# Kernel optimization log

Hardware: AMD Instinct MI355X
Metric: run time of the kernel (lower is better)

The kernel has to match this reference:

```python
import jax, jax.numpy as jnp
import numpy as np

B, L, V, A = 4096, 64, 50000, 1000
E, H, G, F2 = 32, 32, 256, 512


def _xavier(k, shape):
    fan_out, fan_in = shape
    a = np.sqrt(6.0 / (fan_in + fan_out)).astype(np.float32)
    return jax.random.uniform(k, shape, jnp.float32, -a, a)


def setup_inputs() -> dict:
    key = jax.random.key(0)
    ks = jax.random.split(key, 32)
    inp = {}
    inp["q"] = jax.random.randint(ks[0], (B, L), 0, V)
    for i in range(8):
        inp[f"sf{i}"] = jax.random.randint(ks[1 + i], (B, L), 0, V)
    inp["emb"] = _xavier(ks[9], (V, E))
    # torch LSTM weight layout: [4H, in] with gate order i,f,g,o; biases init to 0
    inp["q_Wih"] = _xavier(ks[10], (4 * H, E))
    inp["q_Whh"] = _xavier(ks[11], (4 * H, H))
    inp["q_b"] = jnp.zeros((4 * H,), jnp.float32)
    inp["sf_Wih"] = _xavier(ks[12], (4 * H, E))
    inp["sf_Whh"] = _xavier(ks[13], (4 * H, H))
    inp["sf_b"] = jnp.zeros((4 * H,), jnp.float32)
    inp["g1_W"] = _xavier(ks[14], (G, 2 * H + 1)); inp["g1_b"] = jnp.zeros((G,), jnp.float32)
    inp["g2_W"] = _xavier(ks[15], (G, G)); inp["g2_b"] = jnp.zeros((G,), jnp.float32)
    inp["g3_W"] = _xavier(ks[16], (G, G)); inp["g3_b"] = jnp.zeros((G,), jnp.float32)
    inp["g4_W"] = _xavier(ks[17], (G, G)); inp["g4_b"] = jnp.zeros((G,), jnp.float32)
    inp["f1_W"] = _xavier(ks[18], (G, G)); inp["f1_b"] = jnp.zeros((G,), jnp.float32)
    inp["f2_W"] = _xavier(ks[19], (F2, G)); inp["f2_b"] = jnp.zeros((F2,), jnp.float32)
    inp["f3_W"] = _xavier(ks[20], (A, F2)); inp["f3_b"] = jnp.zeros((A,), jnp.float32)
    return inp


def _lstm_last(x, Wih, Whh, b):
    """x: [L, N, E] -> final hidden state [N, H]. Torch gate order i,f,g,o."""
    n = x.shape[1]
    h_dim = Whh.shape[1]
    def step(carry, xt):
        h, c = carry
        gates = xt @ Wih.T + h @ Whh.T + b  # [N, 4H]
        i, f, g, o = jnp.split(gates, 4, axis=-1)
        c = jax.nn.sigmoid(f) * c + jax.nn.sigmoid(i) * jnp.tanh(g)
        h = jax.nn.sigmoid(o) * jnp.tanh(c)
        return (h, c), None
    init = (jnp.zeros((n, h_dim), x.dtype), jnp.zeros((n, h_dim), x.dtype))
    (h, _), _ = jax.lax.scan(step, init, x)
    return h


def _lin(x, W, b):
    return x @ W.T + b


def reference(q, sf0, sf1, sf2, sf3, sf4, sf5, sf6, sf7,
              emb, q_Wih, q_Whh, q_b, sf_Wih, sf_Whh, sf_b,
              g1_W, g1_b, g2_W, g2_b, g3_W, g3_b, g4_W, g4_b,
              f1_W, f1_b, f2_W, f2_b, f3_W, f3_b):
    # dropout in eval mode (identity)
    b, l = q.shape
    qe = emb[q].transpose(1, 0, 2)  # [L, B, E]
    hq = _lstm_last(qe, q_Wih, q_Whh, q_b)  # [B, H]

    sf = jnp.stack([sf0, sf1, sf2, sf3, sf4, sf5, sf6, sf7])  # [8, B, L]
    sfe = emb[sf]  # [8, B, L, E]
    sfe = sfe.transpose(2, 0, 1, 3).reshape(l, 8 * b, emb.shape[1])  # one fused LSTM over 8*B
    hs = _lstm_last(sfe, sf_Wih, sf_Whh, sf_b).reshape(8, b, -1)  # [8, B, H]

    pos = jnp.broadcast_to(jnp.arange(8, dtype=hs.dtype)[:, None, None], (8, b, 1))
    x = jnp.concatenate([hs, jnp.broadcast_to(hq, (8, b, hq.shape[-1])), pos], axis=-1)  # [8, B, 65]
    x = jax.nn.relu(_lin(x, g1_W, g1_b))
    x = jax.nn.relu(_lin(x, g2_W, g2_b))
    x = jax.nn.relu(_lin(x, g3_W, g3_b))
    x = jax.nn.relu(_lin(x, g4_W, g4_b))
    g_o = x.sum(axis=0)  # [B, 256] segment-sum over the 8 relations

    x = jax.nn.relu(_lin(g_o, f1_W, f1_b))
    x = jax.nn.relu(_lin(x, f2_W, f2_b))
    return _lin(x, f3_W, f3_b)  # [B, A]
```

## Files before the change

kernel.cpp:

```cpp
#include <hip/hip_runtime.h>
#include <stdint.h>
#include <stddef.h>

typedef __fp16 f16;
typedef __attribute__((ext_vector_type(8))) __fp16 half8;
typedef __attribute__((ext_vector_type(4))) __fp16 half4;
typedef __attribute__((ext_vector_type(4))) float f32x4;
typedef unsigned int u32;

static __device__ __forceinline__ f32x4 mfma16(half8 a, half8 b, f32x4 c) {
    return __builtin_amdgcn_mfma_f32_16x16x32_f16(a, b, c, 0, 0, 0);
}
static __device__ __forceinline__ float fexp2(float x) { float r; asm("v_exp_f32 %0, %1" : "=v"(r) : "v"(x)); return r; }
static __device__ __forceinline__ float frcp(float x)  { float r; asm("v_rcp_f32 %0, %1" : "=v"(r) : "v"(x)); return r; }

static constexpr float L2E  = 1.4426950408889634f;
static constexpr float L2E2 = 2.8853900817779268f;

static constexpr int LDA = 264;
static constexpr int LDF2 = 520;

static constexpr size_t OFF_EMB   = 0;
static constexpr size_t OFF_WQIH  = 3200000;
static constexpr size_t OFF_WQHH  = OFF_WQIH + 8192;
static constexpr size_t OFF_WSIH  = OFF_WQHH + 8192;
static constexpr size_t OFF_WSHH  = OFF_WSIH + 8192;
static constexpr size_t OFF_BQ    = OFF_WSHH + 8192;
static constexpr size_t OFF_BS    = OFF_BQ + 512;
static constexpr size_t OFF_G1WP  = OFF_BS + 512;
static constexpr size_t OFF_BIAS8 = OFF_G1WP + 32768;
static constexpr size_t OFF_G2W   = OFF_BIAS8 + 8192;
static constexpr size_t OFF_G3W   = OFF_G2W + 131072;
static constexpr size_t OFF_G4W   = OFF_G3W + 131072;
static constexpr size_t OFF_F1W   = OFF_G4W + 131072;
static constexpr size_t OFF_F2W   = OFF_F1W + 131072;
static constexpr size_t OFF_F3W   = OFF_F2W + 262144;
static constexpr size_t OFF_HS    = OFF_F3W + 1024000;
static constexpr size_t OFF_HQ    = OFF_HS + 2097152;
static constexpr size_t OFF_ACT2  = OFF_HQ + 262144;
static constexpr size_t WS_NEED   = OFF_ACT2 + 16777216;

struct CvtJobs { const float* src[7]; f16* dst[7]; int n[7]; };

__global__ __launch_bounds__(256) void cvt_prep(
    CvtJobs j,
    const float* __restrict__ g1W, const float* __restrict__ g1b,
    f16* __restrict__ wp, float* __restrict__ bias8,
    const float* __restrict__ qWih, const float* __restrict__ qWhh, const float* __restrict__ qb,
    const float* __restrict__ sWih, const float* __restrict__ sWhh, const float* __restrict__ sb,
    f16* __restrict__ wqih, f16* __restrict__ wqhh, float* __restrict__ bq,
    f16* __restrict__ wsih, f16* __restrict__ wshh, float* __restrict__ bs)
{
    int t = threadIdx.x;
    if (blockIdx.y < 7) {
        int jb = blockIdx.y;
        int i = (blockIdx.x * 256 + t) * 8;
        if (i >= j.n[jb]) return;
        const float* s = j.src[jb] + i;
        f32x4 a = *(const f32x4*)s;
        f32x4 b = *(const f32x4*)(s + 4);
        half8 o;
        o[0]=(f16)a[0]; o[1]=(f16)a[1]; o[2]=(f16)a[2]; o[3]=(f16)a[3];
        o[4]=(f16)b[0]; o[5]=(f16)b[1]; o[6]=(f16)b[2]; o[7]=(f16)b[3];
        *(half8*)(j.dst[jb] + i) = o;
        return;
    }
    if (blockIdx.x == 0) {
        int col = t;
        for (int k = 0; k < 64; k++) wp[col * 64 + k] = (f16)g1W[col * 65 + k];
        float wpos = g1W[col * 65 + 64];
        float b = g1b[col];
        for (int i = 0; i < 8; i++) bias8[i * 256 + col] = b + (float)i * wpos;
    } else if (blockIdx.x == 1) {
        for (int i = t; i < 4096; i += 256) {
            int row = i >> 5;
            float s = (row < 64 || row >= 96) ? -L2E : L2E2;
            wqih[i] = (f16)(qWih[i] * s);
            wqhh[i] = (f16)(qWhh[i] * s);
            wsih[i] = (f16)(sWih[i] * s);
            wshh[i] = (f16)(sWhh[i] * s);
        }
        if (t < 128) {
            float s = (t < 64 || t >= 96) ? -L2E : L2E2;
            bq[t] = qb[t] * s;
            bs[t] = sb[t] * s;
        }
    }
}

struct SfPtrs { const int* p[8]; };

__global__ __launch_bounds__(128) void lstm_kernel(
    SfPtrs sf, const int* __restrict__ qtok, const f16* __restrict__ emb_h,
    const f16* __restrict__ wih_sf, const f16* __restrict__ whh_sf, const float* __restrict__ b_sf,
    const f16* __restrict__ wih_q,  const f16* __restrict__ whh_q,  const float* __restrict__ b_q,
    f16* __restrict__ hs_out, f16* __restrict__ hq_out)
{
    __shared__ __align__(16) char hbuf[2][16 * 80];
    int tid = threadIdx.x;
    int w = tid >> 6, lane = tid & 63;
    int c15 = lane & 15, kq = lane >> 4;
    int sbase = blockIdx.x * 16;
    bool isq = sbase >= 32768;
    const f16* wih = isq ? wih_q : wih_sf;
    const f16* whh = isq ? whh_q : whh_sf;
    const float* bvec = isq ? b_q : b_sf;

    half8 wi[4], wh[4];
    f32x4 bc[4];
    #pragma unroll
    for (int jg = 0; jg < 4; jg++) {
        int row = (2 * jg + w) * 16 + c15;
        wi[jg] = *(const half8*)(wih + row * 32 + kq * 8);
        wh[jg] = *(const half8*)(whh + row * 32 + kq * 8);
        bc[jg] = *(const f32x4*)(bvec + (2 * jg + w) * 16 + kq * 4);
    }
    int sg = sbase + c15;
    const int* tp;
    if (isq) tp = qtok + (sg - 32768) * 64;
    else     tp = sf.p[sg >> 12] + (sg & 4095) * 64;

    for (int i = tid; i < 640; i += 128) ((u32*)hbuf[0])[i] = 0;
    __syncthreads();

    float cst[4] = {};
    int rb = 0;
    const int hoff_r = c15 * 80 + kq * 16;
    const int hoff_w = c15 * 80 + w * 32 + kq * 8;

    half8 xf = *(const half8*)(emb_h + (size_t)tp[0] * 32 + kq * 8);

    #pragma unroll 1
    for (int t = 0; t < 64; t++) {
        half8 hf = *(const half8*)(hbuf[rb] + hoff_r);
        f32x4 acc[4];
        #pragma unroll
        for (int jg = 0; jg < 4; jg++) acc[jg] = mfma16(wi[jg], xf, bc[jg]);
        #pragma unroll
        for (int jg = 0; jg < 4; jg++) acc[jg] = mfma16(wh[jg], hf, acc[jg]);
        if (t < 63) {
            int tk = tp[t + 1];
            xf = *(const half8*)(emb_h + (size_t)tk * 32 + kq * 8);
        }
        half4 hp;
        #pragma unroll
        for (int r = 0; r < 4; r++) {
            float ei = fexp2(acc[0][r]);
            float ef = fexp2(acc[1][r]);
            float eg = fexp2(acc[2][r]);
            float eo = fexp2(acc[3][r]);
            float t1 = 1.f + ei, t2 = 1.f + ef, t5 = 1.f + eo;
            float eg1 = eg + 1.f, egm = eg - 1.f;
            float t1e = t1 * eg1;
            float num = fmaf(egm, t2, cst[r] * t1e);
            float cn  = num * frcp(t1e * t2);
            cst[r] = cn;
            float ec  = fexp2(cn * L2E2);
            hp[r] = (f16)((ec - 1.f) * frcp((ec + 1.f) * t5));
        }
        *(half4*)(hbuf[rb ^ 1] + hoff_w) = hp;
        __syncthreads();
        rb ^= 1;
    }
    if (w == 0) {
        half8 hv = *(const half8*)(hbuf[rb] + hoff_r);
        if (isq) *(half8*)(hq_out + (size_t)(sg - 32768) * 32 + kq * 8) = hv;
        else     *(half8*)(hs_out + (size_t)sg * 32 + kq * 8) = hv;
    }
}

template<bool TOGLOBAL>
static __device__ __forceinline__ void layer256(
    const f16 (* __restrict__ src)[LDA], f16 (* __restrict__ dst)[LDA],
    const f16* __restrict__ W, const float* __restrict__ bias,
    f16* __restrict__ gout, int m0, int wm, int wn, int c15, int kq)
{
    f32x4 acc[2][4];
    #pragma unroll
    for (int a = 0; a < 2; a++)
        #pragma unroll
        for (int b = 0; b < 4; b++) acc[a][b] = (f32x4){0.f, 0.f, 0.f, 0.f};
    #pragma unroll
    for (int k0 = 0; k0 < 8; k0++) {
        half8 av[2], bv[4];
        #pragma unroll
        for (int fm = 0; fm < 2; fm++) av[fm] = *(const half8*)(&src[wm * 32 + fm * 16 + c15][k0 * 32 + kq * 8]);
        #pragma unroll
        for (int fn = 0; fn < 4; fn++) bv[fn] = *(const half8*)(W + (size_t)(wn * 64 + fn * 16 + c15) * 256 + k0 * 32 + kq * 8);
        #pragma unroll
        for (int fm = 0; fm < 2; fm++)
            #pragma unroll
            for (int fn = 0; fn < 4; fn++) acc[fm][fn] = mfma16(av[fm], bv[fn], acc[fm][fn]);
    }
    #pragma unroll
    for (int fn = 0; fn < 4; fn++) {
        int col = wn * 64 + fn * 16 + c15;
        float bb = bias[col];
        #pragma unroll
        for (int fm = 0; fm < 2; fm++)
            #pragma unroll
            for (int r = 0; r < 4; r++) {
                float v = fmaxf(acc[fm][fn][r] + bb, 0.f);
                int row = wm * 32 + fm * 16 + kq * 4 + r;
                if (TOGLOBAL) gout[(size_t)(m0 + row) * 256 + col] = (f16)v;
                else          dst[row][col] = (f16)v;
            }
    }
}

__global__ __launch_bounds__(512) void gemm_g1234(
    const f16* __restrict__ hs, const f16* __restrict__ hq,
    const f16* __restrict__ g1wp, const float* __restrict__ bias8,
    const f16* __restrict__ g2w, const float* __restrict__ g2b,
    const f16* __restrict__ g3w, const float* __restrict__ g3b,
    const f16* __restrict__ g4w, const float* __restrict__ g4b,
    f16* __restrict__ act2)
{
    __shared__ __align__(16) f16 actA[64][LDA];
    __shared__ __align__(16) f16 actB[64][LDA];
    const int wv = threadIdx.x >> 6, lane = threadIdx.x & 63;
    const int c15 = lane & 15, kq = lane >> 4;
    const int wm = wv >> 2, wn = wv & 3;
    const int m0 = blockIdx.x * 64;
    const float* brow = bias8 + ((m0 >> 12) << 8);

    {
        f32x4 acc[2][4];
        #pragma unroll
        for (int a = 0; a < 2; a++)
            #pragma unroll
            for (int b = 0; b < 4; b++) acc[a][b] = (f32x4){0.f, 0.f, 0.f, 0.f};
        half8 av[2], bv[4];
        #pragma unroll
        for (int fm = 0; fm < 2; fm++) av[fm] = *(const half8*)(hs + (size_t)(m0 + wm * 32 + fm * 16 + c15) * 32 + kq * 8);
        #pragma unroll
        for (int fn = 0; fn < 4; fn++) bv[fn] = *(const half8*)(g1wp + (size_t)(wn * 64 + fn * 16 + c15) * 64 + kq * 8);
        #pragma unroll
        for (int fm = 0; fm < 2; fm++)
            #pragma unroll
            for (int fn = 0; fn < 4; fn++) acc[fm][fn] = mfma16(av[fm], bv[fn], acc[fm][fn]);
        #pragma unroll
        for (int fm = 0; fm < 2; fm++) av[fm] = *(const half8*)(hq + (size_t)((m0 + wm * 32 + fm * 16 + c15) & 4095) * 32 + kq * 8);
        #pragma unroll
        for (int fn = 0; fn < 4; fn++) bv[fn] = *(const half8*)(g1wp + (size_t)(wn * 64 + fn * 16 + c15) * 64 + 32 + kq * 8);
        #pragma unroll
        for (int fm = 0; fm < 2; fm++)
            #pragma unroll
            for (int fn = 0; fn < 4; fn++) acc[fm][fn] = mfma16(av[fm], bv[fn], acc[fm][fn]);
        #pragma unroll
        for (int fn = 0; fn < 4; fn++) {
            int col = wn * 64 + fn * 16 + c15;
            float bb = brow[col];
            #pragma unroll
            for (int fm = 0; fm < 2; fm++)
                #pragma unroll
                for (int r = 0; r < 4; r++)
                    actA[wm * 32 + fm * 16 + kq * 4 + r][col] = (f16)fmaxf(acc[fm][fn][r] + bb, 0.f);
        }
    }
    __syncthreads();
    layer256<false>(actA, actB, g2w, g2b, nullptr, m0, wm, wn, c15, kq);
    __syncthreads();
    layer256<false>(actB, actA, g3w, g3b, nullptr, m0, wm, wn, c15, kq);
    __syncthreads();
    layer256<true>(actA, actB, g4w, g4b, act2, m0, wm, wn, c15, kq);
}

__global__ __launch_bounds__(512) void f123s_kernel(
    const f16* __restrict__ act2,
    const f16* __restrict__ f1w, const float* __restrict__ f1b,
    const f16* __restrict__ f2w, const float* __restrict__ f2b,
    const f16* __restrict__ f3w, const float* __restrict__ f3b,
    float* __restrict__ out)
{
    __shared__ __align__(16) f16 smbuf[16][LDA];
    __shared__ __align__(16) f16 f1buf[16][LDA];
    __shared__ __align__(16) f16 f2buf[16][LDF2];
    const int b0 = blockIdx.x * 16;

    {
        int r = threadIdx.x >> 5, cb = (threadIdx.x & 31) * 8;
        float s[8] = {};
        #pragma unroll
        for (int i = 0; i < 8; i++) {
            half8 v = *(const half8*)(act2 + ((size_t)(i * 4096 + b0 + r)) * 256 + cb);
            #pragma unroll
            for (int q = 0; q < 8; q++) s[q] += (float)v[q];
        }
        half8 o;
        #pragma unroll
        for (int q = 0; q < 8; q++) o[q] = (f16)s[q];
        *(half8*)(&smbuf[r][cb]) = o;
    }
    __syncthreads();
    const int wv = threadIdx.x >> 6, lane = threadIdx.x & 63;
    const int c15 = lane & 15, kq = lane >> 4;

    {
        f32x4 acc[2];
        acc[0] = (f32x4){0.f, 0.f, 0.f, 0.f}; acc[1] = acc[0];
        #pragma unroll
        for (int k0 = 0; k0 < 8; k0++) {
            half8 a = *(const half8*)(&smbuf[c15][k0 * 32 + kq * 8]);
            #pragma unroll
            for (int fn = 0; fn < 2; fn++) {
                half8 bv = *(const half8*)(f1w + (size_t)(wv * 32 + fn * 16 + c15) * 256 + k0 * 32 + kq * 8);
                acc[fn] = mfma16(a, bv, acc[fn]);
            }
        }
        #pragma unroll
        for (int fn = 0; fn < 2; fn++) {
            int col = wv * 32 + fn * 16 + c15;
            float bb = f1b[col];
            #pragma unroll
            for (int r = 0; r < 4; r++)
                f1buf[kq * 4 + r][col] = (f16)fmaxf(acc[fn][r] + bb, 0.f);
        }
    }
    __syncthreads();
    {
        f32x4 acc[4];
        #pragma unroll
        for (int b = 0; b < 4; b++) acc[b] = (f32x4){0.f, 0.f, 0.f, 0.f};
        #pragma unroll
        for (int k0 = 0; k0 < 8; k0++) {
            half8 a = *(const half8*)(&f1buf[c15][k0 * 32 + kq * 8]);
            #pragma unroll
            for (int fn = 0; fn < 4; fn++) {
                half8 bv = *(const half8*)(f2w + (size_t)(wv * 64 + fn * 16 + c15) * 256 + k0 * 32 + kq * 8);
                acc[fn] = mfma16(a, bv, acc[fn]);
            }
        }
        #pragma unroll
        for (int fn = 0; fn < 4; fn++) {
            int col = wv * 64 + fn * 16 + c15;
            float bb = f2b[col];
            #pragma unroll
            for (int r = 0; r < 4; r++)
                f2buf[kq * 4 + r][col] = (f16)fmaxf(acc[fn][r] + bb, 0.f);
        }
    }
    __syncthreads();
    {
        f32x4 acc[8];
        #pragma unroll
        for (int b = 0; b < 8; b++) acc[b] = (f32x4){0.f, 0.f, 0.f, 0.f};
        #pragma unroll
        for (int k0 = 0; k0 < 16; k0++) {
            half8 a = *(const half8*)(&f2buf[c15][k0 * 32 + kq * 8]);
            #pragma unroll
            for (int fn = 0; fn < 8; fn++) {
                int col = wv * 128 + fn * 16 + c15;
                int cl = col < 1000 ? col : 999;
                half8 bv = *(const half8*)(f3w + (size_t)cl * 512 + k0 * 32 + kq * 8);
                acc[fn] = mfma16(a, bv, acc[fn]);
            }
        }
        #pragma unroll
        for (int fn = 0; fn < 8; fn++) {
            int col = wv * 128 + fn * 16 + c15;
            if (col < 1000) {
                float bb = f3b[col];
                #pragma unroll
                for (int r = 0; r < 4; r++)
                    out[(size_t)(b0 + kq * 4 + r) * 1000 + col] = acc[fn][r] + bb;
            }
        }
    }
}

extern "C" void kernel_launch(void* const* d_in, const int* in_sizes, int n_in,
                              void* d_out, int out_size, void* d_ws, size_t ws_size,
                              hipStream_t stream)
{
    if (ws_size < WS_NEED) return;
    const int* q_tok = (const int*)d_in[0];
    SfPtrs sf;
    for (int i = 0; i < 8; i++) sf.p[i] = (const int*)d_in[1 + i];
    const float* emb_f = (const float*)d_in[9];
    const float* qWih = (const float*)d_in[10];
    const float* qWhh = (const float*)d_in[11];
    const float* q_b  = (const float*)d_in[12];
    const float* sWih = (const float*)d_in[13];
    const float* sWhh = (const float*)d_in[14];
    const float* s_b  = (const float*)d_in[15];
    const float* g1W  = (const float*)d_in[16];
    const float* g1b  = (const float*)d_in[17];
    const float* g2W  = (const float*)d_in[18];
    const float* g2b  = (const float*)d_in[19];
    const float* g3W  = (const float*)d_in[20];
    const float* g3b  = (const float*)d_in[21];
    const float* g4W  = (const float*)d_in[22];
    const float* g4b  = (const float*)d_in[23];
    const float* f1W  = (const float*)d_in[24];
    const float* f1b  = (const float*)d_in[25];
    const float* f2W  = (const float*)d_in[26];
    const float* f2b  = (const float*)d_in[27];
    const float* f3W  = (const float*)d_in[28];
    const float* f3b  = (const float*)d_in[29];

    char* ws = (char*)d_ws;
    f16* emb_h = (f16*)(ws + OFF_EMB);
    f16* wqih  = (f16*)(ws + OFF_WQIH);
    f16* wqhh  = (f16*)(ws + OFF_WQHH);
    f16* wsih  = (f16*)(ws + OFF_WSIH);
    f16* wshh  = (f16*)(ws + OFF_WSHH);
    float* bq  = (float*)(ws + OFF_BQ);
    float* bs  = (float*)(ws + OFF_BS);
    f16* g1wp  = (f16*)(ws + OFF_G1WP);
    float* bias8 = (float*)(ws + OFF_BIAS8);
    f16* g2w = (f16*)(ws + OFF_G2W);
    f16* g3w = (f16*)(ws + OFF_G3W);
    f16* g4w = (f16*)(ws + OFF_G4W);
    f16* f1w = (f16*)(ws + OFF_F1W);
    f16* f2w = (f16*)(ws + OFF_F2W);
    f16* f3w = (f16*)(ws + OFF_F3W);
    f16* hs  = (f16*)(ws + OFF_HS);
    f16* hq  = (f16*)(ws + OFF_HQ);
    f16* act2 = (f16*)(ws + OFF_ACT2);

    CvtJobs cj;
    const float* srcs[7] = {emb_f, g2W, g3W, g4W, f1W, f2W, f3W};
    f16* dsts[7]         = {emb_h, g2w, g3w, g4w, f1w, f2w, f3w};
    int ns[7] = {1600000, 65536, 65536, 65536, 65536, 131072, 512000};
    for (int i = 0; i < 7; i++) { cj.src[i] = srcs[i]; cj.dst[i] = dsts[i]; cj.n[i] = ns[i]; }

    cvt_prep<<<dim3(782, 8), 256, 0, stream>>>(cj, g1W, g1b, g1wp, bias8,
                                               qWih, qWhh, q_b, sWih, sWhh, s_b,
                                               wqih, wqhh, bq, wsih, wshh, bs);
    lstm_kernel<<<2304, 128, 0, stream>>>(sf, q_tok, emb_h, wsih, wshh, bs, wqih, wqhh, bq, hs, hq);
    gemm_g1234<<<512, 512, 0, stream>>>(hs, hq, g1wp, bias8, g2w, g2b, g3w, g3b, g4w, g4b, act2);
    f123s_kernel<<<256, 512, 0, stream>>>(act2, f1w, f1b, f2w, f2b, f3w, f3b, (float*)d_out);
}
```

Baseline: 319.5 us.

## Fuse relation sum into g-MLP kernel by regrouping rows per batch element

The g1-g4 kernel now assigns each block 8 batch elements across all 8 relations, so the segment-sum over relations happens in shared memory and only a [B,256] result goes to global memory instead of the [8B,256] activation buffer. The hq operand is loaded once per block because it is shared across relations. The downstream f1-f3 kernel now reads the pre-summed rows and runs with 1024 threads, splitting each layer's output columns across twice as many waves. Each block's hs loads become strided across relations, and the summed g_o is rounded to fp16 before f1.

```diff
diff --git a/kernel.cpp b/kernel.cpp
--- a/kernel.cpp
+++ b/kernel.cpp
@@ -37,8 +37,8 @@
 static constexpr size_t OFF_F3W   = OFF_F2W + 262144;
 static constexpr size_t OFF_HS    = OFF_F3W + 1024000;
 static constexpr size_t OFF_HQ    = OFF_HS + 2097152;
-static constexpr size_t OFF_ACT2  = OFF_HQ + 262144;
-static constexpr size_t WS_NEED   = OFF_ACT2 + 16777216;
+static constexpr size_t OFF_GO    = OFF_HQ + 262144;
+static constexpr size_t WS_NEED   = OFF_GO + 2097152;
 
 struct CvtJobs { const float* src[7]; f16* dst[7]; int n[7]; };
 
@@ -173,7 +173,7 @@
 static __device__ __forceinline__ void layer256(
     const f16 (* __restrict__ src)[LDA], f16 (* __restrict__ dst)[LDA],
     const f16* __restrict__ W, const float* __restrict__ bias,
-    f16* __restrict__ gout, int m0, int wm, int wn, int c15, int kq)
+    int wm, int wn, int c15, int kq)
 {
     f32x4 acc[2][4];
     #pragma unroll
@@ -201,9 +201,7 @@
             #pragma unroll
             for (int r = 0; r < 4; r++) {
                 float v = fmaxf(acc[fm][fn][r] + bb, 0.f);
-                int row = wm * 32 + fm * 16 + kq * 4 + r;
-                if (TOGLOBAL) gout[(size_t)(m0 + row) * 256 + col] = (f16)v;
-                else          dst[row][col] = (f16)v;
+                dst[wm * 32 + fm * 16 + kq * 4 + r][col] = (f16)v;
             }
     }
 }
@@ -214,15 +212,14 @@
     const f16* __restrict__ g2w, const float* __restrict__ g2b,
     const f16* __restrict__ g3w, const float* __restrict__ g3b,
     const f16* __restrict__ g4w, const float* __restrict__ g4b,
-    f16* __restrict__ act2)
+    f16* __restrict__ go)
 {
     __shared__ __align__(16) f16 actA[64][LDA];
     __shared__ __align__(16) f16 actB[64][LDA];
     const int wv = threadIdx.x >> 6, lane = threadIdx.x & 63;
     const int c15 = lane & 15, kq = lane >> 4;
     const int wm = wv >> 2, wn = wv & 3;
-    const int m0 = blockIdx.x * 64;
-    const float* brow = bias8 + ((m0 >> 12) << 8);
+    const int b8 = blockIdx.x * 8;
 
     {
         f32x4 acc[2][4];
@@ -231,8 +228,13 @@
             #pragma unroll
             for (int b = 0; b < 4; b++) acc[a][b] = (f32x4){0.f, 0.f, 0.f, 0.f};
         half8 av[2], bv[4];
-        #pragma unroll
-        for (int fm = 0; fm < 2; fm++) av[fm] = *(const half8*)(hs + (size_t)(m0 + wm * 32 + fm * 16 + c15) * 32 + kq * 8);
+        half8 avq = *(const half8*)(hq + (size_t)(b8 + (c15 & 7)) * 32 + kq * 8);
+        #pragma unroll
+        for (int fm = 0; fm < 2; fm++) {
+            int l = wm * 32 + fm * 16 + c15;
+            int rowg = (l >> 3) * 4096 + b8 + (l & 7);
+            av[fm] = *(const half8*)(hs + (size_t)rowg * 32 + kq * 8);
+        }
         #pragma unroll
         for (int fn = 0; fn < 4; fn++) bv[fn] = *(const half8*)(g1wp + (size_t)(wn * 64 + fn * 16 + c15) * 64 + kq * 8);
         #pragma unroll
@@ -240,34 +242,45 @@
             #pragma unroll
             for (int fn = 0; fn < 4; fn++) acc[fm][fn] = mfma16(av[fm], bv[fn], acc[fm][fn]);
         #pragma unroll
-        for (int fm = 0; fm < 2; fm++) av[fm] = *(const half8*)(hq + (size_t)((m0 + wm * 32 + fm * 16 + c15) & 4095) * 32 + kq * 8);
-        #pragma unroll
         for (int fn = 0; fn < 4; fn++) bv[fn] = *(const half8*)(g1wp + (size_t)(wn * 64 + fn * 16 + c15) * 64 + 32 + kq * 8);
         #pragma unroll
         for (int fm = 0; fm < 2; fm++)
             #pragma unroll
-            for (int fn = 0; fn < 4; fn++) acc[fm][fn] = mfma16(av[fm], bv[fn], acc[fm][fn]);
+            for (int fn = 0; fn < 4; fn++) acc[fm][fn] = mfma16(avq, bv[fn], acc[fm][fn]);
         #pragma unroll
         for (int fn = 0; fn < 4; fn++) {
             int col = wn * 64 + fn * 16 + c15;
-            float bb = brow[col];
-            #pragma unroll
-            for (int fm = 0; fm < 2; fm++)
+            #pragma unroll
+            for (int fm = 0; fm < 2; fm++) {
+                int rel = wm * 4 + fm * 2 + (kq >> 1);
+                float bb = bias8[rel * 256 + col];
                 #pragma unroll
                 for (int r = 0; r < 4; r++)
                     actA[wm * 32 + fm * 16 + kq * 4 + r][col] = (f16)fmaxf(acc[fm][fn][r] + bb, 0.f);
-        }
-    }
-    __syncthreads();
-    layer256<false>(actA, actB, g2w, g2b, nullptr, m0, wm, wn, c15, kq);
-    __syncthreads();
-    layer256<false>(actB, actA, g3w, g3b, nullptr, m0, wm, wn, c15, kq);
-    __syncthreads();
-    layer256<true>(actA, actB, g4w, g4b, act2, m0, wm, wn, c15, kq);
-}
-
-__global__ __launch_bounds__(512) void f123s_kernel(
-    const f16* __restrict__ act2,
+            }
+        }
+    }
+    __syncthreads();
+    layer256<false>(actA, actB, g2w, g2b, wm, wn, c15, kq);
+    __syncthreads();
+    layer256<false>(actB, actA, g3w, g3b, wm, wn, c15, kq);
+    __syncthreads();
+    layer256<false>(actA, actB, g4w, g4b, wm, wn, c15, kq);
+    __syncthreads();
+    {
+        float s0 = 0.f, s1 = 0.f, s2 = 0.f, s3 = 0.f;
+        #pragma unroll
+        for (int rel = 0; rel < 8; rel++) {
+            half4 v = *(const half4*)(&actB[rel * 8 + wv][lane * 4]);
+            s0 += (float)v[0]; s1 += (float)v[1]; s2 += (float)v[2]; s3 += (float)v[3];
+        }
+        half4 o; o[0] = (f16)s0; o[1] = (f16)s1; o[2] = (f16)s2; o[3] = (f16)s3;
+        *(half4*)(go + (size_t)(b8 + wv) * 256 + lane * 4) = o;
+    }
+}
+
+__global__ __launch_bounds__(1024) void f123s_kernel(
+    const f16* __restrict__ go,
     const f16* __restrict__ f1w, const float* __restrict__ f1b,
     const f16* __restrict__ f2w, const float* __restrict__ f2b,
     const f16* __restrict__ f3w, const float* __restrict__ f3b,
@@ -279,61 +292,46 @@
     const int b0 = blockIdx.x * 16;
 
     {
-        int r = threadIdx.x >> 5, cb = (threadIdx.x & 31) * 8;
-        float s[8] = {};
-        #pragma unroll
-        for (int i = 0; i < 8; i++) {
-            half8 v = *(const half8*)(act2 + ((size_t)(i * 4096 + b0 + r)) * 256 + cb);
-            #pragma unroll
-            for (int q = 0; q < 8; q++) s[q] += (float)v[q];
-        }
-        half8 o;
-        #pragma unroll
-        for (int q = 0; q < 8; q++) o[q] = (f16)s[q];
-        *(half8*)(&smbuf[r][cb]) = o;
+        int t = threadIdx.x;
+        if (t < 512) {
+            int r = t >> 5, cb = (t & 31) * 8;
+            *(half8*)(&smbuf[r][cb]) = *(const half8*)(go + (size_t)(b0 + r) * 256 + cb);
+        }
     }
     __syncthreads();
     const int wv = threadIdx.x >> 6, lane = threadIdx.x & 63;
     const int c15 = lane & 15, kq = lane >> 4;
 
     {
+        f32x4 acc = (f32x4){0.f, 0.f, 0.f, 0.f};
+        #pragma unroll
+        for (int k0 = 0; k0 < 8; k0++) {
+            half8 a = *(const half8*)(&smbuf[c15][k0 * 32 + kq * 8]);
+            half8 bv = *(const half8*)(f1w + (size_t)(wv * 16 + c15) * 256 + k0 * 32 + kq * 8);
+            acc = mfma16(a, bv, acc);
+        }
+        int col = wv * 16 + c15;
+        float bb = f1b[col];
+        #pragma unroll
+        for (int r = 0; r < 4; r++)
+            f1buf[kq * 4 + r][col] = (f16)fmaxf(acc[r] + bb, 0.f);
+    }
+    __syncthreads();
+    {
         f32x4 acc[2];
         acc[0] = (f32x4){0.f, 0.f, 0.f, 0.f}; acc[1] = acc[0];
         #pragma unroll
         for (int k0 = 0; k0 < 8; k0++) {
-            half8 a = *(const half8*)(&smbuf[c15][k0 * 32 + kq * 8]);
+            half8 a = *(const half8*)(&f1buf[c15][k0 * 32 + kq * 8]);
             #pragma unroll
             for (int fn = 0; fn < 2; fn++) {
-                half8 bv = *(const half8*)(f1w + (size_t)(wv * 32 + fn * 16 + c15) * 256 + k0 * 32 + kq * 8);
+                half8 bv = *(const half8*)(f2w + (size_t)(wv * 32 + fn * 16 + c15) * 256 + k0 * 32 + kq * 8);
                 acc[fn] = mfma16(a, bv, acc[fn]);
             }
         }
         #pragma unroll
         for (int fn = 0; fn < 2; fn++) {
             int col = wv * 32 + fn * 16 + c15;
-            float bb = f1b[col];
-            #pragma unroll
-            for (int r = 0; r < 4; r++)
-                f1buf[kq * 4 + r][col] = (f16)fmaxf(acc[fn][r] + bb, 0.f);
-        }
-    }
-    __syncthreads();
-    {
-        f32x4 acc[4];
-        #pragma unroll
-        for (int b = 0; b < 4; b++) acc[b] = (f32x4){0.f, 0.f, 0.f, 0.f};
-        #pragma unroll
-        for (int k0 = 0; k0 < 8; k0++) {
-            half8 a = *(const half8*)(&f1buf[c15][k0 * 32 + kq * 8]);
-            #pragma unroll
-            for (int fn = 0; fn < 4; fn++) {
-                half8 bv = *(const half8*)(f2w + (size_t)(wv * 64 + fn * 16 + c15) * 256 + k0 * 32 + kq * 8);
-                acc[fn] = mfma16(a, bv, acc[fn]);
-            }
-        }
-        #pragma unroll
-        for (int fn = 0; fn < 4; fn++) {
-            int col = wv * 64 + fn * 16 + c15;
             float bb = f2b[col];
             #pragma unroll
             for (int r = 0; r < 4; r++)
@@ -342,23 +340,23 @@
     }
     __syncthreads();
     {
-        f32x4 acc[8];
-        #pragma unroll
-        for (int b = 0; b < 8; b++) acc[b] = (f32x4){0.f, 0.f, 0.f, 0.f};
+        f32x4 acc[4];
+        #pragma unroll
+        for (int b = 0; b < 4; b++) acc[b] = (f32x4){0.f, 0.f, 0.f, 0.f};
         #pragma unroll
         for (int k0 = 0; k0 < 16; k0++) {
             half8 a = *(const half8*)(&f2buf[c15][k0 * 32 + kq * 8]);
             #pragma unroll
-            for (int fn = 0; fn < 8; fn++) {
-                int col = wv * 128 + fn * 16 + c15;
+            for (int fn = 0; fn < 4; fn++) {
+                int col = wv * 64 + fn * 16 + c15;
                 int cl = col < 1000 ? col : 999;
                 half8 bv = *(const half8*)(f3w + (size_t)cl * 512 + k0 * 32 + kq * 8);
                 acc[fn] = mfma16(a, bv, acc[fn]);
             }
         }
         #pragma unroll
-        for (int fn = 0; fn < 8; fn++) {
-            int col = wv * 128 + fn * 16 + c15;
+        for (int fn = 0; fn < 4; fn++) {
+            int col = wv * 64 + fn * 16 + c15;
             if (col < 1000) {
                 float bb = f3b[col];
                 #pragma unroll
@@ -417,7 +415,7 @@
     f16* f3w = (f16*)(ws + OFF_F3W);
     f16* hs  = (f16*)(ws + OFF_HS);
     f16* hq  = (f16*)(ws + OFF_HQ);
-    f16* act2 = (f16*)(ws + OFF_ACT2);
+    f16* go  = (f16*)(ws + OFF_GO);
 
     CvtJobs cj;
     const float* srcs[7] = {emb_f, g2W, g3W, g4W, f1W, f2W, f3W};
@@ -429,6 +427,6 @@
                                                qWih, qWhh, q_b, sWih, sWhh, s_b,
                                                wqih, wqhh, bq, wsih, wshh, bs);
     lstm_kernel<<<2304, 128, 0, stream>>>(sf, q_tok, emb_h, wsih, wshh, bs, wqih, wqhh, bq, hs, hq);
-    gemm_g1234<<<512, 512, 0, stream>>>(hs, hq, g1wp, bias8, g2w, g2b, g3w, g3b, g4w, g4b, act2);
-    f123s_kernel<<<256, 512, 0, stream>>>(act2, f1w, f1b, f2w, f2b, f3w, f3b, (float*)d_out);
-}
+    gemm_g1234<<<512, 512, 0, stream>>>(hs, hq, g1wp, bias8, g2w, g2b, g3w, g3b, g4w, g4b, go);
+    f123s_kernel<<<256, 1024, 0, stream>>>(go, f1w, f1b, f2w, f2b, f3w, f3b, (float*)d_out);
+}
```

Measured after the change: 319.1 us. Within noise of the previous version (-0.1%).
